# Optimization experiments

Measured on AMD Instinct MI355X. Metric: run time of the kernel, lower is better.

The kernel has to match this reference:

```python
import jax, jax.numpy as jnp
import numpy as np

WS = 8   # window_size
SS = 4   # shift_size
NH = 6   # num_heads
EPS = 1e-5


def _win_partition(x, ws):
    # x: [B, H, W, C] -> [B * H/ws * W/ws, ws*ws, C]
    B, H, W, C = x.shape
    x = x.reshape(B, H // ws, ws, W // ws, ws, C)
    return x.transpose(0, 1, 3, 2, 4, 5).reshape(-1, ws * ws, C)


def _win_reverse(wins, ws, H, W, B):
    C = wins.shape[-1]
    x = wins.reshape(B, H // ws, W // ws, ws, ws, C)
    return x.transpose(0, 1, 3, 2, 4, 5).reshape(B, H, W, C)


def _rel_pos_index(ws):
    # static numpy computation, identical to the torch buffer
    coords = np.stack(np.meshgrid(np.arange(ws), np.arange(ws), indexing='ij')).reshape(2, -1)
    rel = coords[:, :, None] - coords[:, None, :]          # [2, N, N]
    rel = rel.transpose(1, 2, 0).copy()                    # [N, N, 2]
    rel[..., 0] += ws - 1
    rel[..., 1] += ws - 1
    rel[..., 0] *= 2 * ws - 1
    return rel.sum(-1)                                     # [N, N] int


def _attn_mask_np(H, W, ws, ss):
    # static numpy computation of the SW-MSA mask, identical to _compute_mask
    img = np.zeros((1, H, W, 1), np.float32)
    cnt = 0
    for hs in (slice(0, -ws), slice(-ws, -ss), slice(-ss, None)):
        for wsl in (slice(0, -ws), slice(-ws, -ss), slice(-ss, None)):
            img[:, hs, wsl, :] = cnt
            cnt += 1
    mw = img.reshape(1, H // ws, ws, W // ws, ws, 1).transpose(0, 1, 3, 2, 4, 5).reshape(-1, ws * ws)
    am = mw[:, None, :] - mw[:, :, None]                   # [nW, N, N]
    return np.where(am != 0, np.float32(-100.0), np.float32(0.0))


def _swin_forward(x, qkv_w, qkv_b, proj_w, proj_b, rpb_table,
                  norm2_g, norm2_b, mlp_w1, mlp_b1, mlp_w2, mlp_b2, H, W):
    B, L, C = x.shape
    ws, ss, nh = WS, SS, NH
    hd = C // nh
    x2d = x.reshape(B, H, W, C)
    shifted = jnp.roll(x2d, (-ss, -ss), axis=(1, 2))
    win = _win_partition(shifted, ws)                      # [B_, N, C]
    B_, N, _ = win.shape

    # --- window attention (note: original applies attention to un-normalized x) ---
    qkv = (win @ qkv_w + qkv_b).reshape(B_, N, 3, nh, hd)
    q = qkv[:, :, 0].transpose(0, 2, 1, 3)                 # [B_, nh, N, hd]
    k = qkv[:, :, 1].transpose(0, 2, 1, 3)
    v = qkv[:, :, 2].transpose(0, 2, 1, 3)
    attn = jnp.einsum('bhnd,bhmd->bhnm', q, k) * (hd ** -0.5)

    bias = rpb_table[jnp.asarray(_rel_pos_index(ws)).reshape(-1)]
    bias = bias.reshape(N, N, nh).transpose(2, 0, 1)       # [nh, N, N]
    attn = attn + bias[None]

    mask = jnp.asarray(_attn_mask_np(H, W, ws, ss))        # [nW, N, N]
    nW = mask.shape[0]
    attn = attn.reshape(B_ // nW, nW, nh, N, N) + mask[None, :, None]
    attn = jax.nn.softmax(attn.reshape(B_, nh, N, N), axis=-1)

    out = jnp.einsum('bhnm,bhmd->bnhd', attn, v).reshape(B_, N, C)
    out = out @ proj_w + proj_b

    x2d = _win_reverse(out, ws, H, W, B)
    x2d = jnp.roll(x2d, (ss, ss), axis=(1, 2))
    x = x + x2d.reshape(B, L, C)

    # --- MLP branch with LayerNorm (norm2) ---
    mu = x.mean(-1, keepdims=True)
    var = x.var(-1, keepdims=True)
    xn = (x - mu) * jax.lax.rsqrt(var + EPS) * norm2_g + norm2_b
    h = jax.nn.gelu(xn @ mlp_w1 + mlp_b1, approximate=False)
    return x + (h @ mlp_w2 + mlp_b2)


def setup_inputs() -> dict:
    B, H, W, C = 8, 128, 128, 192
    mlp_hidden = 4 * C
    ks = jax.random.split(jax.random.key(0), 6)
    std = 0.02
    return {
        'x': jax.random.normal(ks[0], (B, H * W, C), jnp.float32),
        'qkv_w': jax.random.normal(ks[1], (C, 3 * C), jnp.float32) * std,
        'qkv_b': jnp.zeros((3 * C,), jnp.float32),
        'proj_w': jax.random.normal(ks[2], (C, C), jnp.float32) * std,
        'proj_b': jnp.zeros((C,), jnp.float32),
        'rpb_table': jax.random.normal(ks[3], ((2 * WS - 1) ** 2, NH), jnp.float32) * std,
        'norm2_g': jnp.ones((C,), jnp.float32),
        'norm2_b': jnp.zeros((C,), jnp.float32),
        'mlp_w1': jax.random.normal(ks[4], (C, mlp_hidden), jnp.float32) * std,
        'mlp_b1': jnp.zeros((mlp_hidden,), jnp.float32),
        'mlp_w2': jax.random.normal(ks[5], (mlp_hidden, C), jnp.float32) * std,
        'mlp_b2': jnp.zeros((C,), jnp.float32),
        'H': H,
        'W': W,
    }


def reference(x, qkv_w, qkv_b, proj_w, proj_b, rpb_table, norm2_g, norm2_b,
              mlp_w1, mlp_b1, mlp_w2, mlp_b2, H, W):
    return _swin_forward(x, qkv_w, qkv_b, proj_w, proj_b, rpb_table,
                         norm2_g, norm2_b, mlp_w1, mlp_b1, mlp_w2, mlp_b2, H, W)
```

## Files before the change

### kernel.cpp

```cpp
#include <hip/hip_runtime.h>
#include <hip/hip_bf16.h>


typedef __hip_bfloat16 bf16;
typedef __attribute__((ext_vector_type(8))) short bfrag;
typedef __attribute__((ext_vector_type(4))) float ffrag;

union bfu { bf16 h[8]; bfrag v; };

__device__ __forceinline__ float b2f(bf16 v) { return __bfloat162float(v); }
__device__ __forceinline__ bf16  f2b(float v) { return __float2bfloat16(v); }

#define MFMA(a, b, c) __builtin_amdgcn_mfma_f32_16x16x32_bf16((a), (b), (c), 0, 0, 0)

#define WS_XRES  0ULL
#define WS_OG    100663296ULL
#define WS_QKVTG 150994944ULL
#define WS_QBG   151250944ULL
#define WS_PROJT 151253504ULL
#define WS_W1T   151330304ULL
#define WS_W2T   151637504ULL
#define WS_SB    151969280ULL
#define WS_PROJH 152165888ULL

__device__ __forceinline__ void stage_lds(const void* g, void* l, int nbytes, int t) {
    const int lane16 = (t & 63) * 16;
    for (int base = (t >> 6) * 1024; base < nbytes; base += 4096) {
        if (base + lane16 < nbytes) {
            __builtin_amdgcn_global_load_lds(
                (const __attribute__((address_space(1))) void*)((const char*)g + base + lane16),
                (__attribute__((address_space(3))) void*)((char*)l + base),
                16, 0, 0);
        }
    }
}

__device__ __forceinline__ float gelu_t(float x) {
    float y = x * (1.5957691216057308f + 0.07135481627f * x * x);
    return x * (1.f / (1.f + __expf(-y)));
}

__global__ __launch_bounds__(256) void k_prep(
    const float* __restrict__ qkv_w, const float* __restrict__ qkv_b,
    const float* __restrict__ proj_w, const float* __restrict__ w1,
    const float* __restrict__ w2, const float* __restrict__ rpb,
    char* __restrict__ ws)
{
    int i = blockIdx.x * 256 + threadIdx.x;
    bf16*  qkvTg = (bf16*)(ws + WS_QKVTG);
    float* qbg   = (float*)(ws + WS_QBG);
    bf16*  projT = (bf16*)(ws + WS_PROJT);
    bf16*  w1T   = (bf16*)(ws + WS_W1T);
    bf16*  w2T   = (bf16*)(ws + WS_W2T);
    bf16*  sbB   = (bf16*)(ws + WS_SB);
    bf16*  projH = (bf16*)(ws + WS_PROJH);

    if (i < 128000) {
        int g = i / 64000, rem = i % 64000;
        int c = rem / 200, k = rem % 200;
        float v = 0.f;
        if (k < 192 && c < 288) {
            int h = g * 3 + c / 96, j = c % 96;
            int src = (j < 32) ? (h * 32 + j)
                    : (j < 64) ? (192 + h * 32 + (j - 32))
                               : (384 + h * 32 + (j - 64));
            v = qkv_w[k * 576 + src];
        }
        qkvTg[i] = f2b(v);
    } else if (i < 128640) {
        int j = i - 128000;
        int g = j / 320, c = j % 320;
        float v = 0.f;
        if (c < 288) {
            int h = g * 3 + c / 96, jj = c % 96;
            int src = (jj < 32) ? (h * 32 + jj)
                    : (jj < 64) ? (192 + h * 32 + (jj - 32))
                                : (384 + h * 32 + (jj - 64));
            v = qkv_b[src];
        }
        qbg[j] = v;
    } else if (i < 167040) {
        int j = i - 128640;
        int c = j / 200, k = j % 200;
        projT[j] = f2b(k < 192 ? proj_w[k * 192 + c] : 0.f);
    } else if (i < 320640) {
        int j = i - 167040;
        int c = j / 200, k = j % 200;
        w1T[j] = f2b(k < 192 ? w1[k * 768 + c] : 0.f);
    } else if (i < 486528) {
        int j = i - 320640;
        int kc = j / 13824, r = (j % 13824) / 72, kk = j % 72;
        w2T[j] = f2b(kk < 64 ? w2[(kc * 64 + kk) * 192 + r] : 0.f);
    } else if (i < 584832) {
        int j = i - 486528;
        int cls = j / 24576, h = (j % 24576) / 4096;
        int ii = (j % 4096) / 64, jj = j % 64;
        int ri = ii >> 3, ci = ii & 7, rj = jj >> 3, cj = jj & 7;
        float bias = rpb[(((ri - rj + 7) * 15) + (ci - cj + 7)) * 6 + h];
        int clsR = cls >> 1, clsC = cls & 1;
        int regi = (clsR ? (ri < 4 ? 1 : 2) : 0) * 3 + (clsC ? (ci < 4 ? 1 : 2) : 0);
        int regj = (clsR ? (rj < 4 ? 1 : 2) : 0) * 3 + (clsC ? (cj < 4 ? 1 : 2) : 0);
        sbB[j] = f2b(bias + (regi == regj ? 0.f : -100.f));
    } else if (i < 630912) {
        int j = i - 584832;
        int s = j / 7680, c = (j % 7680) / 40, kk = j % 40;
        projH[j] = f2b(kk < 32 ? proj_w[(s * 32 + kk) * 192 + c] : 0.f);
    }
}

__global__ __launch_bounds__(256, 2) void k_attn(
    const float* __restrict__ x, const char* __restrict__ ws,
    const float* __restrict__ proj_b, float* __restrict__ xres)
{
    __shared__ __align__(16) unsigned char smem[67584];
    bf16*  sWb   = (bf16*)(smem);
    bf16*  sQh   = (bf16*)(smem + 25600);
    bf16*  sKh   = (bf16*)(smem + 30720);
    bf16*  sVT   = (bf16*)(smem + 35840);
    bf16*  sP    = (bf16*)(smem + 40448);
    float* sQB   = (float*)(smem + 49664);
    bf16*  sProj = (bf16*)(smem + 52224);

    const bf16*  qkvTg = (const bf16*)(ws + WS_QKVTG);
    const float* qbg   = (const float*)(ws + WS_QBG);
    const bf16*  sbB   = (const bf16*)(ws + WS_SB);
    const bf16*  projH = (const bf16*)(ws + WS_PROJH);

    const int t    = threadIdx.x;
    const int lane = t & 63, quad = lane >> 4, l15 = lane & 15;
    const int wave = t >> 6, r0 = wave * 16;
    const int win = blockIdx.x;
    const int b   = win >> 8;
    const int wi  = win & 255;
    const int wh  = wi >> 4, wwi = wi & 15;

    stage_lds(qbg, smem + 49664, 2560, t);
    stage_lds(qkvTg, sWb, 12800, t);
    stage_lds(projH, sProj, 15360, t);

    bfrag aX[6];
    {
        int row = r0 + l15;
        int rr = row >> 3, cc = row & 7;
        int hs  = (wh * 8 + rr + 4) & 127;
        int wsx = (wwi * 8 + cc + 4) & 127;
        const float* xrow = x + ((size_t)(b * 16384 + hs * 128 + wsx)) * 192;
        #pragma unroll
        for (int kb = 0; kb < 6; kb++) {
            float4 f0 = *(const float4*)(xrow + kb * 32 + quad * 8);
            float4 f1 = *(const float4*)(xrow + kb * 32 + quad * 8 + 4);
            bfu u;
            u.h[0] = f2b(f0.x); u.h[1] = f2b(f0.y); u.h[2] = f2b(f0.z); u.h[3] = f2b(f0.w);
            u.h[4] = f2b(f1.x); u.h[5] = f2b(f1.y); u.h[6] = f2b(f1.z); u.h[7] = f2b(f1.w);
            aX[kb] = u.v;
        }
    }

    size_t tokb[4];
    #pragma unroll
    for (int reg = 0; reg < 4; reg++) {
        int nl = r0 + quad * 4 + reg;
        int sr = wh * 8 + (nl >> 3), sc = wwi * 8 + (nl & 7);
        int h2 = (sr + 4) & 127, w2c = (sc + 4) & 127;
        tokb[reg] = ((size_t)(b * 16384 + h2 * 128 + w2c)) * 192;
    }

    const int cls = ((wh == 15) ? 2 : 0) + ((wwi == 15) ? 1 : 0);
    const bf16* bBc = sbB + (size_t)cls * 24576;
    bf16* sPw = sP + wave * 16 * 72;

    ffrag acc[12];
    #pragma unroll
    for (int ct = 0; ct < 12; ct++)
        acc[ct] = (ffrag){0.f, 0.f, 0.f, 0.f};

    __syncthreads();

    int pb = 0;
    int cb = 0;
    for (int cc = 0; cc < 18; cc++) {
        const int h = cc / 3, cpart = cc - h * 3;
        if (cc < 17) {
            int cbn = (cc == 8) ? 320 : cb + 32;
            stage_lds(qkvTg + (size_t)cbn * 200, sWb + (pb ^ 1) * 6400, 12800, t);
        }
        if (cpart == 1 && cc >= 4)
            stage_lds(projH + (size_t)h * 7680, sProj, 15360, t);

        const bf16* sW = sWb + pb * 6400;
        #pragma unroll
        for (int ct = 0; ct < 2; ct++) {
            bfrag bw[6];
            #pragma unroll
            for (int kb = 0; kb < 6; kb++)
                bw[kb] = *(const bfrag*)&sW[(ct * 16 + l15) * 200 + kb * 32 + quad * 8];
            ffrag qacc = {0.f, 0.f, 0.f, 0.f};
            #pragma unroll
            for (int kb = 0; kb < 6; kb++) qacc = MFMA(aX[kb], bw[kb], qacc);
            float bias = sQB[cb + ct * 16 + l15];
            const int cl = ct * 16 + l15;
            #pragma unroll
            for (int reg = 0; reg < 4; reg++) {
                int r = r0 + quad * 4 + reg;
                float v = qacc[reg] + bias;
                if (cpart == 0)      sQh[r * 40 + cl] = f2b(v);
                else if (cpart == 1) sKh[r * 40 + cl] = f2b(v);
                else                 sVT[cl * 72 + r] = f2b(v);
            }
        }
        __syncthreads();
        pb ^= 1;
        cb = (cc == 8) ? 320 : cb + 32;

        if (cpart == 2) {
            bfrag aQ = *(const bfrag*)&sQh[(r0 + l15) * 40 + quad * 8];
            ffrag Sf[4];
            #pragma unroll
            for (int jt = 0; jt < 4; jt++) {
                bfrag bK = *(const bfrag*)&sKh[(jt * 16 + l15) * 40 + quad * 8];
                ffrag z = {0.f, 0.f, 0.f, 0.f};
                Sf[jt] = MFMA(aQ, bK, z);
            }
            const bf16* bb = bBc + h * 4096 + (r0 + quad * 4) * 64 + l15;
            #pragma unroll
            for (int jt = 0; jt < 4; jt++)
                #pragma unroll
                for (int reg = 0; reg < 4; reg++)
                    Sf[jt][reg] = Sf[jt][reg] * 0.1767766952966369f
                                + b2f(bb[reg * 64 + jt * 16]);
            #pragma unroll
            for (int reg = 0; reg < 4; reg++) {
                float m = fmaxf(fmaxf(Sf[0][reg], Sf[1][reg]), fmaxf(Sf[2][reg], Sf[3][reg]));
                m = fmaxf(m, __shfl_xor(m, 1)); m = fmaxf(m, __shfl_xor(m, 2));
                m = fmaxf(m, __shfl_xor(m, 4)); m = fmaxf(m, __shfl_xor(m, 8));
                float s = 0.f;
                #pragma unroll
                for (int jt = 0; jt < 4; jt++) { Sf[jt][reg] = __expf(Sf[jt][reg] - m); s += Sf[jt][reg]; }
                s += __shfl_xor(s, 1); s += __shfl_xor(s, 2);
                s += __shfl_xor(s, 4); s += __shfl_xor(s, 8);
                float inv = 1.f / s;
                int prow = (quad * 4 + reg) * 72;
                #pragma unroll
                for (int jt = 0; jt < 4; jt++)
                    sPw[prow + jt * 16 + l15] = f2b(Sf[jt][reg] * inv);
            }
            bfrag aP0 = *(const bfrag*)&sPw[l15 * 72 + quad * 8];
            bfrag aP1 = *(const bfrag*)&sPw[l15 * 72 + 32 + quad * 8];
            ffrag o[2];
            #pragma unroll
            for (int ct = 0; ct < 2; ct++) {
                bfrag bV0 = *(const bfrag*)&sVT[(ct * 16 + l15) * 72 + quad * 8];
                bfrag bV1 = *(const bfrag*)&sVT[(ct * 16 + l15) * 72 + 32 + quad * 8];
                ffrag z = {0.f, 0.f, 0.f, 0.f};
                o[ct] = MFMA(aP1, bV1, MFMA(aP0, bV0, z));
            }
            #pragma unroll
            for (int ct = 0; ct < 2; ct++)
                #pragma unroll
                for (int reg = 0; reg < 4; reg++)
                    sPw[(quad * 4 + reg) * 40 + ct * 16 + l15] = f2b(o[ct][reg]);
            bfrag aO = *(const bfrag*)&sPw[l15 * 40 + quad * 8];
            #pragma unroll
            for (int ct2 = 0; ct2 < 12; ct2++) {
                bfrag bwp = *(const bfrag*)&sProj[(ct2 * 16 + l15) * 40 + quad * 8];
                acc[ct2] = MFMA(aO, bwp, acc[ct2]);
            }
            if (cc < 17) __syncthreads();
        }
    }

    #pragma unroll
    for (int ct2 = 0; ct2 < 12; ct2++) {
        int col = ct2 * 16 + l15;
        float pbv = proj_b[col];
        #pragma unroll
        for (int reg = 0; reg < 4; reg++) {
            size_t gi = tokb[reg] + col;
            xres[gi] = acc[ct2][reg] + pbv + x[gi];
        }
    }
}

__global__ __launch_bounds__(256, 2) void k_mlp(
    const float* __restrict__ xres, const float* __restrict__ g,
    const float* __restrict__ bb, const float* __restrict__ b1,
    const float* __restrict__ b2, const char* __restrict__ ws,
    float* __restrict__ out)
{
    __shared__ __align__(16) unsigned char smem[71680];
    bf16* U   = (bf16*)(smem);
    bf16* W2s = (bf16*)(smem + 25600);
    bf16* hS  = (bf16*)(smem + 53248);

    const bf16* w1T = (const bf16*)(ws + WS_W1T);
    const bf16* w2T = (const bf16*)(ws + WS_W2T);

    const int t    = threadIdx.x;
    const int lane = t & 63, quad = lane >> 4, l15 = lane & 15;
    const int wave = t >> 6, r0 = wave * 32;
    const size_t row0 = (size_t)blockIdx.x * 128;

    #pragma unroll
    for (int p = 0; p < 2; p++) {
        int row = r0 + p * 16 + l15;
        const float4* src = (const float4*)(xres + (row0 + row) * 192 + quad * 48);
        float v[48];
        float s = 0.f, sq = 0.f;
        #pragma unroll
        for (int u = 0; u < 12; u++) {
            float4 f = src[u];
            v[u*4] = f.x; v[u*4+1] = f.y; v[u*4+2] = f.z; v[u*4+3] = f.w;
            s  += f.x + f.y + f.z + f.w;
            sq += f.x*f.x + f.y*f.y + f.z*f.z + f.w*f.w;
        }
        s  += __shfl_xor(s, 16);  s  += __shfl_xor(s, 32);
        sq += __shfl_xor(sq, 16); sq += __shfl_xor(sq, 32);
        float mean = s * (1.f / 192.f);
        float var  = sq * (1.f / 192.f) - mean * mean;
        float rstd = rsqrtf(var + 1e-5f);
        __hip_bfloat162* dst = (__hip_bfloat162*)&U[row * 200 + quad * 48];
        #pragma unroll
        for (int u = 0; u < 24; u++) {
            int c = quad * 48 + u * 2;
            float a0 = (v[u*2]   - mean) * rstd * g[c]     + bb[c];
            float a1 = (v[u*2+1] - mean) * rstd * g[c + 1] + bb[c + 1];
            dst[u] = __float22bfloat162_rn({a0, a1});
        }
    }

    bfrag aX[2][6];
    #pragma unroll
    for (int rt = 0; rt < 2; rt++)
        #pragma unroll
        for (int kb = 0; kb < 6; kb++)
            aX[rt][kb] = *(const bfrag*)&U[(r0 + rt*16 + l15) * 200 + kb*32 + quad*8];

    __syncthreads();

    bf16* hs_w = hS + wave * 32 * 72;

    ffrag oacc[2][12];
    #pragma unroll
    for (int rt = 0; rt < 2; rt++)
        #pragma unroll
        for (int ct = 0; ct < 12; ct++)
            oacc[rt][ct] = (ffrag){0.f, 0.f, 0.f, 0.f};

    for (int kc = 0; kc < 12; kc++) {
        __syncthreads();
        stage_lds(w1T + (size_t)kc * 64 * 200, U, 25600, t);
        stage_lds(w2T + (size_t)kc * 13824, W2s, 27648, t);
        __syncthreads();

        #pragma unroll
        for (int ct = 0; ct < 4; ct++) {
            bfrag bw[6];
            #pragma unroll
            for (int kb = 0; kb < 6; kb++)
                bw[kb] = *(const bfrag*)&U[(ct*16 + l15) * 200 + kb*32 + quad*8];
            float bias = b1[kc * 64 + ct * 16 + l15];
            #pragma unroll
            for (int rt = 0; rt < 2; rt++) {
                ffrag a = {0.f, 0.f, 0.f, 0.f};
                #pragma unroll
                for (int kb = 0; kb < 6; kb++) a = MFMA(aX[rt][kb], bw[kb], a);
                #pragma unroll
                for (int reg = 0; reg < 4; reg++)
                    hs_w[(rt*16 + quad*4 + reg) * 72 + ct*16 + l15] =
                        f2b(gelu_t(a[reg] + bias));
            }
        }
        bfrag aH[2][2];
        #pragma unroll
        for (int rt = 0; rt < 2; rt++)
            #pragma unroll
            for (int k0 = 0; k0 < 2; k0++)
                aH[rt][k0] = *(const bfrag*)&hs_w[(rt*16 + l15) * 72 + k0*32 + quad*8];
        #pragma unroll
        for (int ct = 0; ct < 12; ct++) {
            bfrag bw2[2];
            #pragma unroll
            for (int k0 = 0; k0 < 2; k0++)
                bw2[k0] = *(const bfrag*)&W2s[(ct*16 + l15) * 72 + k0*32 + quad*8];
            #pragma unroll
            for (int rt = 0; rt < 2; rt++)
                #pragma unroll
                for (int k0 = 0; k0 < 2; k0++)
                    oacc[rt][ct] = MFMA(aH[rt][k0], bw2[k0], oacc[rt][ct]);
        }
    }

    #pragma unroll
    for (int rt = 0; rt < 2; rt++)
        #pragma unroll
        for (int ct = 0; ct < 12; ct++) {
            int col = ct * 16 + l15;
            float b2v = b2[col];
            #pragma unroll
            for (int reg = 0; reg < 4; reg++) {
                size_t gi = (row0 + r0 + rt*16 + quad*4 + reg) * 192 + col;
                out[gi] = xres[gi] + oacc[rt][ct][reg] + b2v;
            }
        }
}

extern "C" void kernel_launch(void* const* d_in, const int* in_sizes, int n_in,
                              void* d_out, int out_size, void* d_ws, size_t ws_size,
                              hipStream_t stream)
{
    (void)in_sizes; (void)n_in; (void)out_size; (void)ws_size;

    const float* x      = (const float*)d_in[0];
    const float* qkv_w  = (const float*)d_in[1];
    const float* qkv_b  = (const float*)d_in[2];
    const float* proj_w = (const float*)d_in[3];
    const float* proj_b = (const float*)d_in[4];
    const float* rpb    = (const float*)d_in[5];
    const float* n2g    = (const float*)d_in[6];
    const float* n2b    = (const float*)d_in[7];
    const float* w1     = (const float*)d_in[8];
    const float* b1     = (const float*)d_in[9];
    const float* w2     = (const float*)d_in[10];
    const float* b2     = (const float*)d_in[11];

    char*  ws   = (char*)d_ws;
    float* xres = (float*)(ws + WS_XRES);
    float* out  = (float*)d_out;

    hipLaunchKernelGGL(k_prep, dim3(2465), dim3(256), 0, stream,
                       qkv_w, qkv_b, proj_w, w1, w2, rpb, ws);
    hipLaunchKernelGGL(k_attn, dim3(2048), dim3(256), 0, stream,
                       x, ws, proj_b, xres);
    hipLaunchKernelGGL(k_mlp,  dim3(1024), dim3(256), 0, stream,
                       xres, n2g, n2b, b1, b2, ws, out);
}
```

Measured before the change: 470.5 us.

## Read attention weights directly from global memory and shrink LDS for occupancy

The attention kernel no longer stages the QKV weight slices, the QKV bias and the projection weights into shared memory with double buffering. Each wave now loads its MFMA B-fragments straight from global memory, which it expects to hit in L2/L1. This cuts LDS use from about 66 KB to about 24 KB and raises the occupancy hint from 2 to 4 blocks per CU. It also drops one barrier per chunk, but every block re-reads the weights from cache and exposes global-load latency on the MFMA path.

New measurement: 495.7 us. 5.3% more time.

```diff
diff --git a/kernel.cpp b/kernel.cpp
--- a/kernel.cpp
+++ b/kernel.cpp
@@ -108,18 +108,15 @@
     }
 }
 
-__global__ __launch_bounds__(256, 2) void k_attn(
+__global__ __launch_bounds__(256, 4) void k_attn(
     const float* __restrict__ x, const char* __restrict__ ws,
     const float* __restrict__ proj_b, float* __restrict__ xres)
 {
-    __shared__ __align__(16) unsigned char smem[67584];
-    bf16*  sWb   = (bf16*)(smem);
-    bf16*  sQh   = (bf16*)(smem + 25600);
-    bf16*  sKh   = (bf16*)(smem + 30720);
-    bf16*  sVT   = (bf16*)(smem + 35840);
-    bf16*  sP    = (bf16*)(smem + 40448);
-    float* sQB   = (float*)(smem + 49664);
-    bf16*  sProj = (bf16*)(smem + 52224);
+    __shared__ __align__(16) unsigned char smem[24064];
+    bf16* sQh = (bf16*)(smem);
+    bf16* sKh = (bf16*)(smem + 5120);
+    bf16* sVT = (bf16*)(smem + 10240);
+    bf16* sP  = (bf16*)(smem + 14848);
 
     const bf16*  qkvTg = (const bf16*)(ws + WS_QKVTG);
     const float* qbg   = (const float*)(ws + WS_QBG);
@@ -134,10 +131,6 @@
     const int wi  = win & 255;
     const int wh  = wi >> 4, wwi = wi & 15;
 
-    stage_lds(qbg, smem + 49664, 2560, t);
-    stage_lds(qkvTg, sWb, 12800, t);
-    stage_lds(projH, sProj, 15360, t);
-
     bfrag aX[6];
     {
         int row = r0 + l15;
@@ -174,99 +167,91 @@
     for (int ct = 0; ct < 12; ct++)
         acc[ct] = (ffrag){0.f, 0.f, 0.f, 0.f};
 
-    __syncthreads();
-
-    int pb = 0;
-    int cb = 0;
-    for (int cc = 0; cc < 18; cc++) {
-        const int h = cc / 3, cpart = cc - h * 3;
-        if (cc < 17) {
-            int cbn = (cc == 8) ? 320 : cb + 32;
-            stage_lds(qkvTg + (size_t)cbn * 200, sWb + (pb ^ 1) * 6400, 12800, t);
-        }
-        if (cpart == 1 && cc >= 4)
-            stage_lds(projH + (size_t)h * 7680, sProj, 15360, t);
-
-        const bf16* sW = sWb + pb * 6400;
+    for (int h = 0; h < 6; h++) {
+        const int g = h / 3, hl = h - g * 3;
+        const int hbase = g * 320 + hl * 96;
+
+        #pragma unroll
+        for (int cpart = 0; cpart < 3; cpart++) {
+            const int cb = hbase + cpart * 32;
+            #pragma unroll
+            for (int ct = 0; ct < 2; ct++) {
+                const bf16* wsrc = qkvTg + (size_t)(cb + ct * 16 + l15) * 200 + quad * 8;
+                bfrag bw[6];
+                #pragma unroll
+                for (int kb = 0; kb < 6; kb++)
+                    bw[kb] = *(const bfrag*)(wsrc + kb * 32);
+                ffrag qacc = {0.f, 0.f, 0.f, 0.f};
+                #pragma unroll
+                for (int kb = 0; kb < 6; kb++) qacc = MFMA(aX[kb], bw[kb], qacc);
+                float bias = qbg[cb + ct * 16 + l15];
+                const int cl = ct * 16 + l15;
+                #pragma unroll
+                for (int reg = 0; reg < 4; reg++) {
+                    int r = r0 + quad * 4 + reg;
+                    float v = qacc[reg] + bias;
+                    if (cpart == 0)      sQh[r * 40 + cl] = f2b(v);
+                    else if (cpart == 1) sKh[r * 40 + cl] = f2b(v);
+                    else                 sVT[cl * 72 + r] = f2b(v);
+                }
+            }
+        }
+        __syncthreads();
+
+        bfrag aQ = *(const bfrag*)&sQh[(r0 + l15) * 40 + quad * 8];
+        ffrag Sf[4];
+        #pragma unroll
+        for (int jt = 0; jt < 4; jt++) {
+            bfrag bK = *(const bfrag*)&sKh[(jt * 16 + l15) * 40 + quad * 8];
+            ffrag z = {0.f, 0.f, 0.f, 0.f};
+            Sf[jt] = MFMA(aQ, bK, z);
+        }
+        const bf16* bb = bBc + h * 4096 + (r0 + quad * 4) * 64 + l15;
+        #pragma unroll
+        for (int jt = 0; jt < 4; jt++)
+            #pragma unroll
+            for (int reg = 0; reg < 4; reg++)
+                Sf[jt][reg] = Sf[jt][reg] * 0.1767766952966369f
+                            + b2f(bb[reg * 64 + jt * 16]);
+        #pragma unroll
+        for (int reg = 0; reg < 4; reg++) {
+            float m = fmaxf(fmaxf(Sf[0][reg], Sf[1][reg]), fmaxf(Sf[2][reg], Sf[3][reg]));
+            m = fmaxf(m, __shfl_xor(m, 1)); m = fmaxf(m, __shfl_xor(m, 2));
+            m = fmaxf(m, __shfl_xor(m, 4)); m = fmaxf(m, __shfl_xor(m, 8));
+            float s = 0.f;
+            #pragma unroll
+            for (int jt = 0; jt < 4; jt++) { Sf[jt][reg] = __expf(Sf[jt][reg] - m); s += Sf[jt][reg]; }
+            s += __shfl_xor(s, 1); s += __shfl_xor(s, 2);
+            s += __shfl_xor(s, 4); s += __shfl_xor(s, 8);
+            float inv = 1.f / s;
+            int prow = (quad * 4 + reg) * 72;
+            #pragma unroll
+            for (int jt = 0; jt < 4; jt++)
+                sPw[prow + jt * 16 + l15] = f2b(Sf[jt][reg] * inv);
+        }
+        bfrag aP0 = *(const bfrag*)&sPw[l15 * 72 + quad * 8];
+        bfrag aP1 = *(const bfrag*)&sPw[l15 * 72 + 32 + quad * 8];
+        ffrag o[2];
         #pragma unroll
         for (int ct = 0; ct < 2; ct++) {
-            bfrag bw[6];
-            #pragma unroll
-            for (int kb = 0; kb < 6; kb++)
-                bw[kb] = *(const bfrag*)&sW[(ct * 16 + l15) * 200 + kb * 32 + quad * 8];
-            ffrag qacc = {0.f, 0.f, 0.f, 0.f};
-            #pragma unroll
-            for (int kb = 0; kb < 6; kb++) qacc = MFMA(aX[kb], bw[kb], qacc);
-            float bias = sQB[cb + ct * 16 + l15];
-            const int cl = ct * 16 + l15;
-            #pragma unroll
-            for (int reg = 0; reg < 4; reg++) {
-                int r = r0 + quad * 4 + reg;
-                float v = qacc[reg] + bias;
-                if (cpart == 0)      sQh[r * 40 + cl] = f2b(v);
-                else if (cpart == 1) sKh[r * 40 + cl] = f2b(v);
-                else                 sVT[cl * 72 + r] = f2b(v);
-            }
-        }
-        __syncthreads();
-        pb ^= 1;
-        cb = (cc == 8) ? 320 : cb + 32;
-
-        if (cpart == 2) {
-            bfrag aQ = *(const bfrag*)&sQh[(r0 + l15) * 40 + quad * 8];
-            ffrag Sf[4];
-            #pragma unroll
-            for (int jt = 0; jt < 4; jt++) {
-                bfrag bK = *(const bfrag*)&sKh[(jt * 16 + l15) * 40 + quad * 8];
-                ffrag z = {0.f, 0.f, 0.f, 0.f};
-                Sf[jt] = MFMA(aQ, bK, z);
-            }
-            const bf16* bb = bBc + h * 4096 + (r0 + quad * 4) * 64 + l15;
-            #pragma unroll
-            for (int jt = 0; jt < 4; jt++)
-                #pragma unroll
-                for (int reg = 0; reg < 4; reg++)
-                    Sf[jt][reg] = Sf[jt][reg] * 0.1767766952966369f
-                                + b2f(bb[reg * 64 + jt * 16]);
-            #pragma unroll
-            for (int reg = 0; reg < 4; reg++) {
-                float m = fmaxf(fmaxf(Sf[0][reg], Sf[1][reg]), fmaxf(Sf[2][reg], Sf[3][reg]));
-                m = fmaxf(m, __shfl_xor(m, 1)); m = fmaxf(m, __shfl_xor(m, 2));
-                m = fmaxf(m, __shfl_xor(m, 4)); m = fmaxf(m, __shfl_xor(m, 8));
-                float s = 0.f;
-                #pragma unroll
-                for (int jt = 0; jt < 4; jt++) { Sf[jt][reg] = __expf(Sf[jt][reg] - m); s += Sf[jt][reg]; }
-                s += __shfl_xor(s, 1); s += __shfl_xor(s, 2);
-                s += __shfl_xor(s, 4); s += __shfl_xor(s, 8);
-                float inv = 1.f / s;
-                int prow = (quad * 4 + reg) * 72;
-                #pragma unroll
-                for (int jt = 0; jt < 4; jt++)
-                    sPw[prow + jt * 16 + l15] = f2b(Sf[jt][reg] * inv);
-            }
-            bfrag aP0 = *(const bfrag*)&sPw[l15 * 72 + quad * 8];
-            bfrag aP1 = *(const bfrag*)&sPw[l15 * 72 + 32 + quad * 8];
-            ffrag o[2];
-            #pragma unroll
-            for (int ct = 0; ct < 2; ct++) {
-                bfrag bV0 = *(const bfrag*)&sVT[(ct * 16 + l15) * 72 + quad * 8];
-                bfrag bV1 = *(const bfrag*)&sVT[(ct * 16 + l15) * 72 + 32 + quad * 8];
-                ffrag z = {0.f, 0.f, 0.f, 0.f};
-                o[ct] = MFMA(aP1, bV1, MFMA(aP0, bV0, z));
-            }
-            #pragma unroll
-            for (int ct = 0; ct < 2; ct++)
-                #pragma unroll
-                for (int reg = 0; reg < 4; reg++)
-                    sPw[(quad * 4 + reg) * 40 + ct * 16 + l15] = f2b(o[ct][reg]);
-            bfrag aO = *(const bfrag*)&sPw[l15 * 40 + quad * 8];
-            #pragma unroll
-            for (int ct2 = 0; ct2 < 12; ct2++) {
-                bfrag bwp = *(const bfrag*)&sProj[(ct2 * 16 + l15) * 40 + quad * 8];
-                acc[ct2] = MFMA(aO, bwp, acc[ct2]);
-            }
-            if (cc < 17) __syncthreads();
-        }
+            bfrag bV0 = *(const bfrag*)&sVT[(ct * 16 + l15) * 72 + quad * 8];
+            bfrag bV1 = *(const bfrag*)&sVT[(ct * 16 + l15) * 72 + 32 + quad * 8];
+            ffrag z = {0.f, 0.f, 0.f, 0.f};
+            o[ct] = MFMA(aP1, bV1, MFMA(aP0, bV0, z));
+        }
+        #pragma unroll
+        for (int ct = 0; ct < 2; ct++)
+            #pragma unroll
+            for (int reg = 0; reg < 4; reg++)
+                sPw[(quad * 4 + reg) * 40 + ct * 16 + l15] = f2b(o[ct][reg]);
+        bfrag aO = *(const bfrag*)&sPw[l15 * 40 + quad * 8];
+        const bf16* psrc = projH + (size_t)h * 7680 + (size_t)l15 * 40 + quad * 8;
+        #pragma unroll
+        for (int ct2 = 0; ct2 < 12; ct2++) {
+            bfrag bwp = *(const bfrag*)(psrc + ct2 * 640);
+            acc[ct2] = MFMA(aO, bwp, acc[ct2]);
+        }
+        if (h < 5) __syncthreads();
     }
 
     #pragma unroll
```

## Process two windows per attention block and share staged QKV weights

Applied to the files above, without the earlier changes.

The attention kernel now runs 512 threads and handles two windows per block, so each double-buffered QKV weight tile staged into LDS is shared by eight waves instead of four. This halves the block count and the per-window weight staging traffic. The projection weights and QKV bias are no longer staged into LDS; they are read directly from global memory (relying on cache), which removes the per-head proj staging. The cost is more global loads in the inner projection loop and a larger LDS footprint per block, which may limit occupancy.

Result: slower. 514.1 us (+9.3%).

```diff
diff --git a/kernel.cpp b/kernel.cpp
--- a/kernel.cpp
+++ b/kernel.cpp
@@ -26,6 +26,18 @@
 __device__ __forceinline__ void stage_lds(const void* g, void* l, int nbytes, int t) {
     const int lane16 = (t & 63) * 16;
     for (int base = (t >> 6) * 1024; base < nbytes; base += 4096) {
+        if (base + lane16 < nbytes) {
+            __builtin_amdgcn_global_load_lds(
+                (const __attribute__((address_space(1))) void*)((const char*)g + base + lane16),
+                (__attribute__((address_space(3))) void*)((char*)l + base),
+                16, 0, 0);
+        }
+    }
+}
+
+__device__ __forceinline__ void stage_lds8(const void* g, void* l, int nbytes, int t) {
+    const int lane16 = (t & 63) * 16;
+    for (int base = (t >> 6) * 1024; base < nbytes; base += 8192) {
         if (base + lane16 < nbytes) {
             __builtin_amdgcn_global_load_lds(
                 (const __attribute__((address_space(1))) void*)((const char*)g + base + lane16),
@@ -108,18 +120,12 @@
     }
 }
 
-__global__ __launch_bounds__(256, 2) void k_attn(
+__global__ __launch_bounds__(512, 2) void k_attn(
     const float* __restrict__ x, const char* __restrict__ ws,
     const float* __restrict__ proj_b, float* __restrict__ xres)
 {
-    __shared__ __align__(16) unsigned char smem[67584];
-    bf16*  sWb   = (bf16*)(smem);
-    bf16*  sQh   = (bf16*)(smem + 25600);
-    bf16*  sKh   = (bf16*)(smem + 30720);
-    bf16*  sVT   = (bf16*)(smem + 35840);
-    bf16*  sP    = (bf16*)(smem + 40448);
-    float* sQB   = (float*)(smem + 49664);
-    bf16*  sProj = (bf16*)(smem + 52224);
+    __shared__ __align__(16) unsigned char smem[73728];
+    bf16* sWb = (bf16*)(smem);
 
     const bf16*  qkvTg = (const bf16*)(ws + WS_QKVTG);
     const float* qbg   = (const float*)(ws + WS_QBG);
@@ -128,15 +134,20 @@
 
     const int t    = threadIdx.x;
     const int lane = t & 63, quad = lane >> 4, l15 = lane & 15;
-    const int wave = t >> 6, r0 = wave * 16;
-    const int win = blockIdx.x;
-    const int b   = win >> 8;
-    const int wi  = win & 255;
-    const int wh  = wi >> 4, wwi = wi & 15;
-
-    stage_lds(qbg, smem + 49664, 2560, t);
-    stage_lds(qkvTg, sWb, 12800, t);
-    stage_lds(projH, sProj, 15360, t);
+    const int wave = t >> 6;
+    const int ww   = wave >> 2;
+    const int r0   = (wave & 3) * 16;
+    const int win  = blockIdx.x * 2 + ww;
+    const int b    = win >> 8;
+    const int wi   = win & 255;
+    const int wh   = wi >> 4, wwi = wi & 15;
+
+    bf16* sQh = (bf16*)(smem + 25600 + ww * 5120);
+    bf16* sKh = (bf16*)(smem + 35840 + ww * 5120);
+    bf16* sVT = (bf16*)(smem + 46080 + ww * 4608);
+    bf16* sPw = (bf16*)(smem + 55296 + wave * 2304);
+
+    stage_lds8(qkvTg, sWb, 12800, t);
 
     bfrag aX[6];
     {
@@ -167,7 +178,6 @@
 
     const int cls = ((wh == 15) ? 2 : 0) + ((wwi == 15) ? 1 : 0);
     const bf16* bBc = sbB + (size_t)cls * 24576;
-    bf16* sPw = sP + wave * 16 * 72;
 
     ffrag acc[12];
     #pragma unroll
@@ -182,11 +192,8 @@
         const int h = cc / 3, cpart = cc - h * 3;
         if (cc < 17) {
             int cbn = (cc == 8) ? 320 : cb + 32;
-            stage_lds(qkvTg + (size_t)cbn * 200, sWb + (pb ^ 1) * 6400, 12800, t);
-        }
-        if (cpart == 1 && cc >= 4)
-            stage_lds(projH + (size_t)h * 7680, sProj, 15360, t);
-
+            stage_lds8(qkvTg + (size_t)cbn * 200, sWb + (pb ^ 1) * 6400, 12800, t);
+        }
         const bf16* sW = sWb + pb * 6400;
         #pragma unroll
         for (int ct = 0; ct < 2; ct++) {
@@ -197,7 +204,7 @@
             ffrag qacc = {0.f, 0.f, 0.f, 0.f};
             #pragma unroll
             for (int kb = 0; kb < 6; kb++) qacc = MFMA(aX[kb], bw[kb], qacc);
-            float bias = sQB[cb + ct * 16 + l15];
+            float bias = qbg[cb + ct * 16 + l15];
             const int cl = ct * 16 + l15;
             #pragma unroll
             for (int reg = 0; reg < 4; reg++) {
@@ -260,9 +267,10 @@
                 for (int reg = 0; reg < 4; reg++)
                     sPw[(quad * 4 + reg) * 40 + ct * 16 + l15] = f2b(o[ct][reg]);
             bfrag aO = *(const bfrag*)&sPw[l15 * 40 + quad * 8];
+            const bf16* psrc = projH + (size_t)h * 7680 + (size_t)l15 * 40 + quad * 8;
             #pragma unroll
             for (int ct2 = 0; ct2 < 12; ct2++) {
-                bfrag bwp = *(const bfrag*)&sProj[(ct2 * 16 + l15) * 40 + quad * 8];
+                bfrag bwp = *(const bfrag*)(psrc + ct2 * 640);
                 acc[ct2] = MFMA(aO, bwp, acc[ct2]);
             }
             if (cc < 17) __syncthreads();
@@ -429,7 +437,7 @@
 
     hipLaunchKernelGGL(k_prep, dim3(2465), dim3(256), 0, stream,
                        qkv_w, qkv_b, proj_w, w1, w2, rpb, ws);
-    hipLaunchKernelGGL(k_attn, dim3(2048), dim3(256), 0, stream,
+    hipLaunchKernelGGL(k_attn, dim3(1024), dim3(512), 0, stream,
                        x, ws, proj_b, xres);
     hipLaunchKernelGGL(k_mlp,  dim3(1024), dim3(256), 0, stream,
                        xres, n2g, n2b, b1, b2, ws, out);
```
